# Performance work log

Measured on AMD Instinct MI355X. Metric: run time of the kernel, lower is better.

## Reference

```python
import jax, jax.numpy as jnp
import numpy as np

DIM = 512
WIN = 7
HEADS = 16
N = WIN * WIN            # 49 tokens per window
NW = 64                  # windows per image (56/7)^2
BATCH = 32               # images
B_ = BATCH * NW          # 2048 window-batches
TABLE = (2 * WIN - 1) ** 2  # 169


def _relative_position_index(win):
    # Faithful to the TF construction in __init__.
    coords = np.stack(np.meshgrid(np.arange(win), np.arange(win), indexing='ij'))
    coords = coords.reshape(2, -1).T                      # [N, 2]
    rel = coords[:, None, :] - coords[None, :, :]          # [N, N, 2]
    rel = rel + (win - 1)
    idx = rel[..., 0] * (2 * win - 1) + rel[..., 1]        # [N, N]
    return jnp.asarray(idx, dtype=jnp.int32)


def setup_inputs() -> dict:
    key = jax.random.key(0)
    ks = jax.random.split(key, 7)
    x = jax.random.normal(ks[0], (B_, N, DIM), dtype=jnp.float32)
    # shifted-window additive mask: 0 where allowed, -100 where blocked
    mask = jnp.where(jax.random.uniform(ks[1], (NW, N, N)) < 0.8, 0.0, -100.0).astype(jnp.float32)
    qkv_w = jax.random.normal(ks[2], (DIM, 3 * DIM), dtype=jnp.float32) * 0.02
    qkv_b = jax.random.normal(ks[3], (3 * DIM,), dtype=jnp.float32) * 0.02
    proj_w = jax.random.normal(ks[4], (DIM, DIM), dtype=jnp.float32) * 0.02
    proj_b = jax.random.normal(ks[5], (DIM,), dtype=jnp.float32) * 0.02
    rel_table = jax.random.normal(ks[6], (TABLE, HEADS), dtype=jnp.float32) * 0.02
    rel_index = _relative_position_index(WIN)
    return {"x": x, "mask": mask, "qkv_w": qkv_w, "qkv_b": qkv_b,
            "proj_w": proj_w, "proj_b": proj_b,
            "rel_table": rel_table, "rel_index": rel_index}


def reference(x, mask, qkv_w, qkv_b, proj_w, proj_b, rel_table, rel_index):
    B, n, C = x.shape
    hd = C // HEADS
    scale = hd ** (-0.5)
    # qkv projection -> [3, B, H, N, hd]
    qkv = (x @ qkv_w + qkv_b).reshape(B, n, 3, HEADS, hd).transpose(2, 0, 3, 1, 4)
    q, k, v = qkv[0] * scale, qkv[1], qkv[2]
    attn = jnp.einsum('bhnd,bhmd->bhnm', q, k)             # [B, H, N, N]
    # relative position bias gather: [N*N] -> [N, N, H] -> [H, N, N]
    bias = rel_table[rel_index.reshape(-1)].reshape(n, n, HEADS).transpose(2, 0, 1)
    attn = attn + bias[None]
    nW = mask.shape[0]
    attn = attn.reshape(B // nW, nW, HEADS, n, n) + mask[None, :, None]
    attn = attn.reshape(-1, HEADS, n, n)
    attn = jax.nn.softmax(attn, axis=-1)
    out = jnp.einsum('bhnm,bhmd->bhnd', attn, v)           # [B, H, N, hd]
    out = out.transpose(0, 2, 1, 3).reshape(B, n, C)
    return out @ proj_w + proj_b
```

## Files before the change

kernel.cpp:

```cpp
#include <hip/hip_runtime.h>

typedef unsigned short ushort_t;
typedef short short8 __attribute__((ext_vector_type(8)));
typedef float f32x4 __attribute__((ext_vector_type(4)));
typedef unsigned short ushort4v __attribute__((ext_vector_type(4)));

__device__ __forceinline__ ushort_t f2bf(float f) {
    unsigned int u = __float_as_uint(f);
    u = (u + 0x7fffu + ((u >> 16) & 1u)) >> 16;
    return (ushort_t)u;
}

__device__ __forceinline__ void async16(void* lds, const void* g) {
    __builtin_amdgcn_global_load_lds(
        (const __attribute__((address_space(1))) unsigned int*)g,
        (__attribute__((address_space(3))) unsigned int*)lds, 16, 0, 0);
}

__global__ void conv_x_kernel(const float* __restrict__ in, ushort_t* __restrict__ out) {
    int i = blockIdx.x * 256 + threadIdx.x;
    float4 v = ((const float4*)in)[i];
    ushort4v o;
    o.x = f2bf(v.x); o.y = f2bf(v.y); o.z = f2bf(v.z); o.w = f2bf(v.w);
    ((ushort4v*)out)[i] = o;
}

__global__ void prep_weights(const float* __restrict__ qkv_w, const float* __restrict__ proj_w,
                             ushort_t* __restrict__ wtq, ushort_t* __restrict__ wtp) {
    int o = blockIdx.x * 256 + threadIdx.x;
    if (o < 1536 * 512) {
        int n = o >> 9, k = o & 511;
        wtq[o] = f2bf(qkv_w[k * 1536 + n]);
    }
    if (o < 512 * 512) {
        int n = o >> 9, k = o & 511;
        wtp[o] = f2bf(proj_w[k * 512 + n]);
    }
}

__global__ void build_cm(const float* __restrict__ mask, const float* __restrict__ rel_table,
                         const int* __restrict__ rel_index, float* __restrict__ cm) {
    int o = blockIdx.x * 256 + threadIdx.x;
    int c = o & 63, r = (o >> 6) & 63, h = (o >> 12) & 15, w = o >> 16;
    float v = -30000.0f;
    if (r < 49 && c < 49)
        v = rel_table[rel_index[r * 49 + c] * 16 + h] + mask[w * 2401 + r * 49 + c];
    cm[o] = v;
}


#define STAGE(ldsbase, gbase) do {                                              \
    _Pragma("unroll")                                                           \
    for (int j_ = 0; j_ < 2; ++j_) {                                            \
        const int idx_ = j_ * 512 + tid;                                        \
        const int row_ = idx_ >> 3;                                             \
        const int sc_  = (((idx_ & 7) ^ (row_ & 7)) << 3);                      \
        async16((char*)(ldsbase) + idx_ * 16, (gbase) + (size_t)row_ * K + sc_);\
    }                                                                           \
} while (0)

#define VMNOP ((void)0)
#define VM0 asm volatile("s_waitcnt vmcnt(0)" ::: "memory")
#define NOSTAGE ((void)0)

#define PHASE(buf, mh, nh, WAITST, ...) do {                                    \
    short8 af_[4][2], bf_[2][2];                                                \
    _Pragma("unroll")                                                           \
    for (int f_ = 0; f_ < 4; ++f_) {                                            \
        const int ar_ = wr + ((mh) * 4 + f_) * 16 + lr;                         \
        _Pragma("unroll")                                                       \
        for (int ks_ = 0; ks_ < 2; ++ks_)                                       \
            af_[f_][ks_] = *(const short8*)&As[buf][ar_ * 64 + ((ks_ * 32 + lk * 8) ^ ((ar_ & 7) << 3))]; \
    }                                                                           \
    _Pragma("unroll")                                                           \
    for (int g_ = 0; g_ < 2; ++g_) {                                            \
        const int br_ = wc + ((nh) * 2 + g_) * 16 + lr;                         \
        _Pragma("unroll")                                                       \
        for (int ks_ = 0; ks_ < 2; ++ks_)                                       \
            bf_[g_][ks_] = *(const short8*)&Bs[buf][br_ * 64 + ((ks_ * 32 + lk * 8) ^ ((br_ & 7) << 3))]; \
    }                                                                           \
    __VA_ARGS__;                                                                \
    __builtin_amdgcn_s_barrier();                                               \
    asm volatile("s_waitcnt lgkmcnt(0)" ::: "memory");                          \
    __builtin_amdgcn_sched_barrier(0);                                          \
    __builtin_amdgcn_s_setprio(1);                                              \
    _Pragma("unroll")                                                           \
    for (int f_ = 0; f_ < 4; ++f_)                                              \
        _Pragma("unroll")                                                       \
        for (int g_ = 0; g_ < 2; ++g_)                                          \
            _Pragma("unroll")                                                   \
            for (int ks_ = 0; ks_ < 2; ++ks_)                                   \
                acc[(mh) * 4 + f_][(nh) * 2 + g_] = __builtin_amdgcn_mfma_f32_16x16x32_bf16( \
                    bf_[g_][ks_], af_[f_][ks_], acc[(mh) * 4 + f_][(nh) * 2 + g_], 0, 0, 0); \
    __builtin_amdgcn_s_setprio(0);                                              \
    WAITST;                                                                     \
    __builtin_amdgcn_s_barrier();                                               \
} while (0)

template<int NB_N, int NSTR, bool QKV, int K>
__global__ __launch_bounds__(512, 2)
void gemm8(const ushort_t* __restrict__ A, const ushort_t* __restrict__ Bt,
           const float* __restrict__ bias, void* __restrict__ out)
{
    __shared__ alignas(16) ushort_t As[2][256 * 64];
    __shared__ alignas(16) ushort_t Bs[2][256 * 64];

    const int tid = threadIdx.x;
    const int wid = tid >> 6, lane = tid & 63;
    const int lr = lane & 15, lk = lane >> 4;
    const int wr = (wid >> 2) * 128;
    const int wc = (wid & 3) * 64;

    const int chunk = gridDim.x >> 3;
    const int wg = ((int)blockIdx.x & 7) * chunk + ((int)blockIdx.x >> 3);
    const int nb = wg % NB_N;
    const int mb = wg / NB_N;
    const int m0 = mb << 8, n0 = nb << 8;

    const size_t a0 = (size_t)m0 * K;
    const size_t a1 = (size_t)(m0 + 128) * K;
    const size_t b0 = (size_t)n0 * K;
    const size_t b1 = (size_t)(n0 + 128) * K;

    f32x4 acc[8][4];
#pragma unroll
    for (int f = 0; f < 8; ++f)
#pragma unroll
        for (int g = 0; g < 4; ++g)
#pragma unroll
            for (int r = 0; r < 4; ++r) acc[f][g][r] = 0.f;

    STAGE(&As[0][0],    A  + a0);
    STAGE(&As[0][8192], A  + a1);
    STAGE(&Bs[0][0],    Bt + b0);
    STAGE(&Bs[0][8192], Bt + b1);
    VM0;
    __builtin_amdgcn_s_barrier();

    const int NI = K >> 7;
    for (int i = 0; i < NI; ++i) {
        const int ck = (2 * i + 1) << 6;
        const int cn = (2 * i + 2) << 6;
        const bool more = (i < NI - 1);
        PHASE(0, 0, 0, VMNOP, { STAGE(&As[1][0], A + a0 + ck); STAGE(&As[1][8192], A + a1 + ck); });
        PHASE(0, 0, 1, VMNOP, { STAGE(&Bs[1][0], Bt + b0 + ck); STAGE(&Bs[1][8192], Bt + b1 + ck); });
        PHASE(0, 1, 0, VMNOP, NOSTAGE);
        PHASE(0, 1, 1, VM0,   NOSTAGE);
        PHASE(1, 0, 0, VMNOP, { if (more) { STAGE(&As[0][0], A + a0 + cn); STAGE(&As[0][8192], A + a1 + cn); } });
        PHASE(1, 0, 1, VMNOP, { if (more) { STAGE(&Bs[0][0], Bt + b0 + cn); STAGE(&Bs[0][8192], Bt + b1 + cn); } });
        PHASE(1, 1, 0, VMNOP, NOSTAGE);
        PHASE(1, 1, 1, VM0,   NOSTAGE);
    }

#pragma unroll
    for (int f = 0; f < 8; ++f) {
        const int row = m0 + wr + f * 16 + lr;
#pragma unroll
        for (int g = 0; g < 4; ++g) {
            const int col = n0 + wc + g * 16 + lk * 4;
            const float4 bv = *(const float4*)&bias[col];
            float v0 = acc[f][g][0] + bv.x;
            float v1 = acc[f][g][1] + bv.y;
            float v2 = acc[f][g][2] + bv.z;
            float v3 = acc[f][g][3] + bv.w;
            if (QKV) {
                if (col < 512) {
                    v0 *= 0.17677669529663689f; v1 *= 0.17677669529663689f;
                    v2 *= 0.17677669529663689f; v3 *= 0.17677669529663689f;
                }
                ushort4v o;
                o.x = f2bf(v0); o.y = f2bf(v1); o.z = f2bf(v2); o.w = f2bf(v3);
                *(ushort4v*)&((ushort_t*)out)[(size_t)row * NSTR + col] = o;
            } else {
                float4 o; o.x = v0; o.y = v1; o.z = v2; o.w = v3;
                *(float4*)&((float*)out)[(size_t)row * NSTR + col] = o;
            }
        }
    }
}

#define PL_STRIDE 80
#define VT_STRIDE 88
__global__ __launch_bounds__(256, 2)
void attn_kernel(const ushort_t* __restrict__ qkv, const float* __restrict__ cm,
                 ushort_t* __restrict__ out)
{
    __shared__ alignas(16) char smem[4 * 64 * PL_STRIDE * 2 + 4 * 32 * VT_STRIDE * 2];
    float* cmf = (float*)smem;
    ushort_t* Pl = (ushort_t*)smem;
    ushort_t* vT = (ushort_t*)(smem + 4 * 64 * PL_STRIDE * 2);

    const int w = blockIdx.x, h = blockIdx.y, ig = blockIdx.z;
    const int tid = threadIdx.x;
    const int wid = tid >> 6, lane = tid & 63;
    const int lr = lane & 15, lk = lane >> 4;
    const int b = (ig * 4 + wid) * 64 + w;

    const float* cmsrc = cm + ((size_t)(w * 16 + h) << 12);
    for (int t = tid; t < 4096; t += 256)
        cmf[(t >> 6) * 65 + (t & 63)] = cmsrc[t];
    __syncthreads();

    const size_t base = (size_t)b * 49 * 1536 + h * 32;

    short8 aq[4], bk[4];
#pragma unroll
    for (int i = 0; i < 4; ++i) {
        int n = i * 16 + lr; n = n > 48 ? 48 : n;
        aq[i] = *(const short8*)&qkv[base + (size_t)n * 1536 + lk * 8];
    }
#pragma unroll
    for (int j = 0; j < 4; ++j) {
        int m = j * 16 + lr; m = m > 48 ? 48 : m;
        bk[j] = *(const short8*)&qkv[base + 512 + (size_t)m * 1536 + lk * 8];
    }

    f32x4 s[4][4];
#pragma unroll
    for (int i = 0; i < 4; ++i)
#pragma unroll
        for (int j = 0; j < 4; ++j)
#pragma unroll
            for (int r = 0; r < 4; ++r) s[i][j][r] = 0.f;
#pragma unroll
    for (int i = 0; i < 4; ++i)
#pragma unroll
        for (int j = 0; j < 4; ++j)
            s[i][j] = __builtin_amdgcn_mfma_f32_16x16x32_bf16(aq[i], bk[j], s[i][j], 0, 0, 0);

    short8 vv[4];
#pragma unroll
    for (int t = 0; t < 4; ++t)
#pragma unroll
        for (int e = 0; e < 8; ++e) vv[t][e] = 0;
    if (lane < 49) {
        const ushort_t* vp = &qkv[base + 1024 + (size_t)lane * 1536];
#pragma unroll
        for (int t = 0; t < 4; ++t) vv[t] = *(const short8*)(vp + t * 8);
    }
    ushort_t* vTw = vT + wid * 32 * VT_STRIDE;
#pragma unroll
    for (int t = 0; t < 4; ++t)
#pragma unroll
        for (int e = 0; e < 8; ++e)
            vTw[(t * 8 + e) * VT_STRIDE + lane] = (ushort_t)vv[t][e];

#pragma unroll
    for (int i = 0; i < 4; ++i) {
#pragma unroll
        for (int r = 0; r < 4; ++r) {
            const int row = i * 16 + lk * 4 + r;
            float v0 = s[i][0][r] + cmf[row * 65 + lr];
            float v1 = s[i][1][r] + cmf[row * 65 + 16 + lr];
            float v2 = s[i][2][r] + cmf[row * 65 + 32 + lr];
            float v3 = s[i][3][r] + cmf[row * 65 + 48 + lr];
            float mx = fmaxf(fmaxf(v0, v1), fmaxf(v2, v3));
#pragma unroll
            for (int t = 1; t < 16; t <<= 1) mx = fmaxf(mx, __shfl_xor(mx, t, 64));
            v0 = __expf(v0 - mx); v1 = __expf(v1 - mx);
            v2 = __expf(v2 - mx); v3 = __expf(v3 - mx);
            float sm = v0 + v1 + v2 + v3;
#pragma unroll
            for (int t = 1; t < 16; t <<= 1) sm += __shfl_xor(sm, t, 64);
            const float inv = 1.0f / sm;
            s[i][0][r] = v0 * inv; s[i][1][r] = v1 * inv;
            s[i][2][r] = v2 * inv; s[i][3][r] = v3 * inv;
        }
    }
    __syncthreads();

    ushort_t* Pw = Pl + wid * 64 * PL_STRIDE;
#pragma unroll
    for (int i = 0; i < 4; ++i)
#pragma unroll
        for (int j = 0; j < 4; ++j)
#pragma unroll
            for (int r = 0; r < 4; ++r)
                Pw[(i * 16 + lk * 4 + r) * PL_STRIDE + j * 16 + lr] = f2bf(s[i][j][r]);

    f32x4 o[4][2];
#pragma unroll
    for (int i = 0; i < 4; ++i)
#pragma unroll
        for (int jb = 0; jb < 2; ++jb)
#pragma unroll
            for (int r = 0; r < 4; ++r) o[i][jb][r] = 0.f;
#pragma unroll
    for (int ks = 0; ks < 2; ++ks) {
        short8 pa[4], vb[2];
#pragma unroll
        for (int i = 0; i < 4; ++i)
            pa[i] = *(const short8*)&Pw[(i * 16 + lr) * PL_STRIDE + ks * 32 + lk * 8];
#pragma unroll
        for (int jb = 0; jb < 2; ++jb)
            vb[jb] = *(const short8*)&vTw[(jb * 16 + lr) * VT_STRIDE + ks * 32 + lk * 8];
#pragma unroll
        for (int i = 0; i < 4; ++i)
#pragma unroll
            for (int jb = 0; jb < 2; ++jb)
                o[i][jb] = __builtin_amdgcn_mfma_f32_16x16x32_bf16(vb[jb], pa[i], o[i][jb], 0, 0, 0);
    }

    const size_t obase = (size_t)b * 49 * 512 + h * 32;
#pragma unroll
    for (int i = 0; i < 4; ++i) {
        const int n = i * 16 + lr;
        if (n < 49) {
#pragma unroll
            for (int jb = 0; jb < 2; ++jb) {
                ushort4v ov;
                ov.x = f2bf(o[i][jb][0]); ov.y = f2bf(o[i][jb][1]);
                ov.z = f2bf(o[i][jb][2]); ov.w = f2bf(o[i][jb][3]);
                *(ushort4v*)&out[obase + (size_t)n * 512 + jb * 16 + lk * 4] = ov;
            }
        }
    }
}

extern "C" void kernel_launch(void* const* d_in, const int* in_sizes, int n_in,
                              void* d_out, int out_size, void* d_ws, size_t ws_size,
                              hipStream_t stream)
{
    const float* x         = (const float*)d_in[0];
    const float* mask      = (const float*)d_in[1];
    const float* qkv_w     = (const float*)d_in[2];
    const float* qkv_b     = (const float*)d_in[3];
    const float* proj_w    = (const float*)d_in[4];
    const float* proj_b    = (const float*)d_in[5];
    const float* rel_table = (const float*)d_in[6];
    const int*   rel_index = (const int*)d_in[7];

    char* ws = (char*)d_ws;
    ushort_t* xb  = (ushort_t*)ws;
    ushort_t* qkv = (ushort_t*)(ws + 102760448);
    ushort_t* wtq = (ushort_t*)(ws + 411041792);
    ushort_t* wtp = (ushort_t*)(ws + 412614656);
    float*    cm  = (float*)  (ws + 413138944);

    conv_x_kernel<<<50176, 256, 0, stream>>>(x, xb);
    prep_weights<<<3072, 256, 0, stream>>>(qkv_w, proj_w, wtq, wtp);
    build_cm<<<16384, 256, 0, stream>>>(mask, rel_table, rel_index, cm);

    gemm8<6, 1536, true, 512><<<2352, 512, 0, stream>>>(xb, wtq, qkv_b, qkv);

    attn_kernel<<<dim3(64, 16, 8), 256, 0, stream>>>(qkv, cm, xb);

    gemm8<2, 512, false, 512><<<784, 512, 0, stream>>>(xb, wtp, proj_b, d_out);
}
```

Measured before the change: 656.6 us.

## Restructure GEMM inner loop into two half-tile phases with all staging up front

Replaces the four quarter-tile phases per K-slice with two half-tile phases. B fragments for all four column groups are loaded once and reused across both M halves, and all four global-to-LDS stages for the next K-slice are issued together at the start of each tile. This cuts barriers and repeated B fragment reads per K step. In exchange it uses more registers for fragments and gives the async copies less spread-out issue across phases.

```diff
diff --git a/kernel.cpp b/kernel.cpp
--- a/kernel.cpp
+++ b/kernel.cpp
@@ -59,41 +59,62 @@
     }                                                                           \
 } while (0)
 
-#define VMNOP ((void)0)
 #define VM0 asm volatile("s_waitcnt vmcnt(0)" ::: "memory")
-#define NOSTAGE ((void)0)
-
-#define PHASE(buf, mh, nh, WAITST, ...) do {                                    \
-    short8 af_[4][2], bf_[2][2];                                                \
+
+#define LOADA(buf, mh) do {                                                     \
     _Pragma("unroll")                                                           \
     for (int f_ = 0; f_ < 4; ++f_) {                                            \
         const int ar_ = wr + ((mh) * 4 + f_) * 16 + lr;                         \
         _Pragma("unroll")                                                       \
         for (int ks_ = 0; ks_ < 2; ++ks_)                                       \
-            af_[f_][ks_] = *(const short8*)&As[buf][ar_ * 64 + ((ks_ * 32 + lk * 8) ^ ((ar_ & 7) << 3))]; \
+            af[f_][ks_] = *(const short8*)&As[buf][ar_ * 64 + ((ks_ * 32 + lk * 8) ^ ((ar_ & 7) << 3))]; \
     }                                                                           \
+} while (0)
+
+#define LOADB(buf) do {                                                         \
     _Pragma("unroll")                                                           \
-    for (int g_ = 0; g_ < 2; ++g_) {                                            \
-        const int br_ = wc + ((nh) * 2 + g_) * 16 + lr;                         \
+    for (int g_ = 0; g_ < 4; ++g_) {                                            \
+        const int br_ = wc + g_ * 16 + lr;                                      \
         _Pragma("unroll")                                                       \
         for (int ks_ = 0; ks_ < 2; ++ks_)                                       \
-            bf_[g_][ks_] = *(const short8*)&Bs[buf][br_ * 64 + ((ks_ * 32 + lk * 8) ^ ((br_ & 7) << 3))]; \
+            bf[g_][ks_] = *(const short8*)&Bs[buf][br_ * 64 + ((ks_ * 32 + lk * 8) ^ ((br_ & 7) << 3))]; \
     }                                                                           \
-    __VA_ARGS__;                                                                \
+} while (0)
+
+#define WAITLDS do {                                                            \
     __builtin_amdgcn_s_barrier();                                               \
     asm volatile("s_waitcnt lgkmcnt(0)" ::: "memory");                          \
     __builtin_amdgcn_sched_barrier(0);                                          \
+} while (0)
+
+#define MFMAH(mh) do {                                                          \
     __builtin_amdgcn_s_setprio(1);                                              \
     _Pragma("unroll")                                                           \
     for (int f_ = 0; f_ < 4; ++f_)                                              \
         _Pragma("unroll")                                                       \
-        for (int g_ = 0; g_ < 2; ++g_)                                          \
+        for (int g_ = 0; g_ < 4; ++g_)                                          \
             _Pragma("unroll")                                                   \
             for (int ks_ = 0; ks_ < 2; ++ks_)                                   \
-                acc[(mh) * 4 + f_][(nh) * 2 + g_] = __builtin_amdgcn_mfma_f32_16x16x32_bf16( \
-                    bf_[g_][ks_], af_[f_][ks_], acc[(mh) * 4 + f_][(nh) * 2 + g_], 0, 0, 0); \
+                acc[(mh) * 4 + f_][g_] = __builtin_amdgcn_mfma_f32_16x16x32_bf16( \
+                    bf[g_][ks_], af[f_][ks_], acc[(mh) * 4 + f_][g_], 0, 0, 0); \
     __builtin_amdgcn_s_setprio(0);                                              \
-    WAITST;                                                                     \
+} while (0)
+
+#define TILE(buf, DOSTAGE, koff) do {                                           \
+    short8 af[4][2], bf[4][2];                                                  \
+    LOADB(buf); LOADA(buf, 0);                                                  \
+    if (DOSTAGE) {                                                              \
+        STAGE(&As[(buf) ^ 1][0],    A  + a0 + (koff));                          \
+        STAGE(&As[(buf) ^ 1][8192], A  + a1 + (koff));                          \
+        STAGE(&Bs[(buf) ^ 1][0],    Bt + b0 + (koff));                          \
+        STAGE(&Bs[(buf) ^ 1][8192], Bt + b1 + (koff));                          \
+    }                                                                           \
+    WAITLDS;                                                                    \
+    MFMAH(0);                                                                   \
+    LOADA(buf, 1);       \
+    WAITLDS;                                                                    \
+    MFMAH(1);                                                                   \
+    VM0;                      \
     __builtin_amdgcn_s_barrier();                                               \
 } while (0)
 
@@ -137,19 +158,12 @@
     VM0;
     __builtin_amdgcn_s_barrier();
 
-    const int NI = K >> 7;
-    for (int i = 0; i < NI; ++i) {
-        const int ck = (2 * i + 1) << 6;
-        const int cn = (2 * i + 2) << 6;
-        const bool more = (i < NI - 1);
-        PHASE(0, 0, 0, VMNOP, { STAGE(&As[1][0], A + a0 + ck); STAGE(&As[1][8192], A + a1 + ck); });
-        PHASE(0, 0, 1, VMNOP, { STAGE(&Bs[1][0], Bt + b0 + ck); STAGE(&Bs[1][8192], Bt + b1 + ck); });
-        PHASE(0, 1, 0, VMNOP, NOSTAGE);
-        PHASE(0, 1, 1, VM0,   NOSTAGE);
-        PHASE(1, 0, 0, VMNOP, { if (more) { STAGE(&As[0][0], A + a0 + cn); STAGE(&As[0][8192], A + a1 + cn); } });
-        PHASE(1, 0, 1, VMNOP, { if (more) { STAGE(&Bs[0][0], Bt + b0 + cn); STAGE(&Bs[0][8192], Bt + b1 + cn); } });
-        PHASE(1, 1, 0, VMNOP, NOSTAGE);
-        PHASE(1, 1, 1, VM0,   NOSTAGE);
+    const int KT = K >> 6;
+    for (int t = 0; t < KT; t += 2) {
+        const int c1 = (t + 1) << 6;
+        const int c2 = (t + 2) << 6;
+        TILE(0, true,          c1);
+        TILE(1, (t + 2 < KT),  c2);
     }
 
 #pragma unroll
```

Measured after the change: 643.9 us. Within noise of the previous version (-1.9%).

## Split GEMM K-tiles into half-tiles with deeper async prefetch pipeline

Applied to the files above, without the earlier changes.

Restructures the bf16 GEMM main loop so each 64-wide K tile is staged as two 32-wide halves in a four-slot ring, with loads issued three half-tiles ahead and partial vmcnt(8) waits in place of full drains. Each phase now covers a full 4x4 fragment block for one K half, reusing the B fragments across two phases, and uses a new XOR swizzle suited to 32-element rows. The aim is to keep more global-to-LDS transfers in flight and reduce stalls at barriers. The cost is more complex wait accounting, with a risk of correctness or hazard problems if the vmcnt counts are off, and smaller MFMA bursts per barrier.

```diff
diff --git a/kernel.cpp b/kernel.cpp
--- a/kernel.cpp
+++ b/kernel.cpp
@@ -49,37 +49,35 @@
 }
 
 
-#define STAGE(ldsbase, gbase) do {                                              \
+#define STAGEH(ldsbase, gbase) do {                                             \
     _Pragma("unroll")                                                           \
     for (int j_ = 0; j_ < 2; ++j_) {                                            \
         const int idx_ = j_ * 512 + tid;                                        \
-        const int row_ = idx_ >> 3;                                             \
-        const int sc_  = (((idx_ & 7) ^ (row_ & 7)) << 3);                      \
-        async16((char*)(ldsbase) + idx_ * 16, (gbase) + (size_t)row_ * K + sc_);\
+        const int row_ = idx_ >> 2;                                             \
+        const int sw_  = (idx_ & 3) ^ ((row_ >> 1) & 3);                        \
+        async16((char*)(ldsbase) + idx_ * 16, (gbase) + (size_t)row_ * K + sw_ * 8); \
     }                                                                           \
 } while (0)
 
-#define VMNOP ((void)0)
+#define VM8 asm volatile("s_waitcnt vmcnt(8)" ::: "memory")
 #define VM0 asm volatile("s_waitcnt vmcnt(0)" ::: "memory")
-#define NOSTAGE ((void)0)
-
-#define PHASE(buf, mh, nh, WAITST, ...) do {                                    \
-    short8 af_[4][2], bf_[2][2];                                                \
+#define NOSTG ((void)0)
+
+#define PH(AB, BB, mh, LOADBF, STG, VMW) do {                                   \
+    if (LOADBF) {                                                               \
+        _Pragma("unroll")                                                       \
+        for (int g_ = 0; g_ < 4; ++g_) {                                        \
+            const int br_ = wc + g_ * 16 + lr;                                  \
+            bf[g_] = *(const short8*)&(BB)[br_ * 32 + ((lk ^ ((br_ >> 1) & 3)) << 3)]; \
+        }                                                                       \
+    }                                                                           \
     _Pragma("unroll")                                                           \
     for (int f_ = 0; f_ < 4; ++f_) {                                            \
-        const int ar_ = wr + ((mh) * 4 + f_) * 16 + lr;                         \
-        _Pragma("unroll")                                                       \
-        for (int ks_ = 0; ks_ < 2; ++ks_)                                       \
-            af_[f_][ks_] = *(const short8*)&As[buf][ar_ * 64 + ((ks_ * 32 + lk * 8) ^ ((ar_ & 7) << 3))]; \
+        const int ar_ = wr + (mh) * 64 + f_ * 16 + lr;                          \
+        af[f_] = *(const short8*)&(AB)[ar_ * 32 + ((lk ^ ((ar_ >> 1) & 3)) << 3)]; \
     }                                                                           \
-    _Pragma("unroll")                                                           \
-    for (int g_ = 0; g_ < 2; ++g_) {                                            \
-        const int br_ = wc + ((nh) * 2 + g_) * 16 + lr;                         \
-        _Pragma("unroll")                                                       \
-        for (int ks_ = 0; ks_ < 2; ++ks_)                                       \
-            bf_[g_][ks_] = *(const short8*)&Bs[buf][br_ * 64 + ((ks_ * 32 + lk * 8) ^ ((br_ & 7) << 3))]; \
-    }                                                                           \
-    __VA_ARGS__;                                                                \
+    STG;                                                                        \
+    VMW;                                                                        \
     __builtin_amdgcn_s_barrier();                                               \
     asm volatile("s_waitcnt lgkmcnt(0)" ::: "memory");                          \
     __builtin_amdgcn_sched_barrier(0);                                          \
@@ -87,13 +85,10 @@
     _Pragma("unroll")                                                           \
     for (int f_ = 0; f_ < 4; ++f_)                                              \
         _Pragma("unroll")                                                       \
-        for (int g_ = 0; g_ < 2; ++g_)                                          \
-            _Pragma("unroll")                                                   \
-            for (int ks_ = 0; ks_ < 2; ++ks_)                                   \
-                acc[(mh) * 4 + f_][(nh) * 2 + g_] = __builtin_amdgcn_mfma_f32_16x16x32_bf16( \
-                    bf_[g_][ks_], af_[f_][ks_], acc[(mh) * 4 + f_][(nh) * 2 + g_], 0, 0, 0); \
+        for (int g_ = 0; g_ < 4; ++g_)                                          \
+            acc[(mh) * 4 + f_][g_] = __builtin_amdgcn_mfma_f32_16x16x32_bf16(   \
+                bf[g_], af[f_], acc[(mh) * 4 + f_][g_], 0, 0, 0);               \
     __builtin_amdgcn_s_setprio(0);                                              \
-    WAITST;                                                                     \
     __builtin_amdgcn_s_barrier();                                               \
 } while (0)
 
@@ -102,8 +97,8 @@
 void gemm8(const ushort_t* __restrict__ A, const ushort_t* __restrict__ Bt,
            const float* __restrict__ bias, void* __restrict__ out)
 {
-    __shared__ alignas(16) ushort_t As[2][256 * 64];
-    __shared__ alignas(16) ushort_t Bs[2][256 * 64];
+    __shared__ alignas(16) ushort_t As[2][2][256 * 32];
+    __shared__ alignas(16) ushort_t Bs[2][2][256 * 32];
 
     const int tid = threadIdx.x;
     const int wid = tid >> 6, lane = tid & 63;
@@ -117,10 +112,8 @@
     const int mb = wg / NB_N;
     const int m0 = mb << 8, n0 = nb << 8;
 
-    const size_t a0 = (size_t)m0 * K;
-    const size_t a1 = (size_t)(m0 + 128) * K;
-    const size_t b0 = (size_t)n0 * K;
-    const size_t b1 = (size_t)(n0 + 128) * K;
+    const size_t am = (size_t)m0 * K;
+    const size_t bm = (size_t)n0 * K;
 
     f32x4 acc[8][4];
 #pragma unroll
@@ -130,26 +123,37 @@
 #pragma unroll
             for (int r = 0; r < 4; ++r) acc[f][g][r] = 0.f;
 
-    STAGE(&As[0][0],    A  + a0);
-    STAGE(&As[0][8192], A  + a1);
-    STAGE(&Bs[0][0],    Bt + b0);
-    STAGE(&Bs[0][8192], Bt + b1);
-    VM0;
+    STAGEH(&As[0][0][0], A  + am);
+    STAGEH(&Bs[0][0][0], Bt + bm);
+    STAGEH(&As[0][1][0], A  + am + 32);
+    STAGEH(&Bs[0][1][0], Bt + bm + 32);
+    STAGEH(&As[1][0][0], A  + am + 64);
+    STAGEH(&Bs[1][0][0], Bt + bm + 64);
+    VM8;
     __builtin_amdgcn_s_barrier();
 
     const int NI = K >> 7;
     for (int i = 0; i < NI; ++i) {
-        const int ck = (2 * i + 1) << 6;
-        const int cn = (2 * i + 2) << 6;
+        const int t = 2 * i;
         const bool more = (i < NI - 1);
-        PHASE(0, 0, 0, VMNOP, { STAGE(&As[1][0], A + a0 + ck); STAGE(&As[1][8192], A + a1 + ck); });
-        PHASE(0, 0, 1, VMNOP, { STAGE(&Bs[1][0], Bt + b0 + ck); STAGE(&Bs[1][8192], Bt + b1 + ck); });
-        PHASE(0, 1, 0, VMNOP, NOSTAGE);
-        PHASE(0, 1, 1, VM0,   NOSTAGE);
-        PHASE(1, 0, 0, VMNOP, { if (more) { STAGE(&As[0][0], A + a0 + cn); STAGE(&As[0][8192], A + a1 + cn); } });
-        PHASE(1, 0, 1, VMNOP, { if (more) { STAGE(&Bs[0][0], Bt + b0 + cn); STAGE(&Bs[0][8192], Bt + b1 + cn); } });
-        PHASE(1, 1, 0, VMNOP, NOSTAGE);
-        PHASE(1, 1, 1, VM0,   NOSTAGE);
+        short8 af[4], bf[4];
+        PH(As[0][0], Bs[0][0], 0, true,
+           STAGEH(&As[1][1][0], A  + am + (size_t)(t + 1) * 64 + 32), VM8);
+        PH(As[0][0], Bs[0][0], 1, false,
+           STAGEH(&Bs[1][1][0], Bt + bm + (size_t)(t + 1) * 64 + 32), VM8);
+        PH(As[0][1], Bs[0][1], 0, true,
+           if (more) STAGEH(&As[0][0][0], A  + am + (size_t)(t + 2) * 64), VM8);
+        PH(As[0][1], Bs[0][1], 1, false,
+           if (more) STAGEH(&Bs[0][0][0], Bt + bm + (size_t)(t + 2) * 64), VM8);
+        PH(As[1][0], Bs[1][0], 0, true,
+           if (more) STAGEH(&As[0][1][0], A  + am + (size_t)(t + 2) * 64 + 32), VM8);
+        PH(As[1][0], Bs[1][0], 1, false,
+           if (more) STAGEH(&Bs[0][1][0], Bt + bm + (size_t)(t + 2) * 64 + 32),
+           do { if (more) { VM8; } else { VM0; } } while (0));
+        PH(As[1][1], Bs[1][1], 0, true,
+           if (more) STAGEH(&As[1][0][0], A  + am + (size_t)(t + 3) * 64), VM8);
+        PH(As[1][1], Bs[1][1], 1, false,
+           if (more) STAGEH(&Bs[1][0][0], Bt + bm + (size_t)(t + 3) * 64), VM8);
     }
 
 #pragma unroll
```

New measurement: 648.6 us. No clear change (-1.2%).
